# Performance work log

Hardware: AMD Instinct MI355X
Metric: run time of the kernel (lower is better)

Reference implementation:

```python
import jax, jax.numpy as jnp
import numpy as np

K = 256            # number of learned permutations (config['k'])
N = 256            # nb_experts
NOISE_FACTOR = 0.01
TAU_INITIAL = 1e-3
TAU_FINAL = 1e-7
N_ITERS_MIN, N_ITERS_MAX = 20, 150
ITERS_TOTAL = 100 * 1000   # epochs_for_learning_permutation * steps_per_epoch
EPS = 1e-20


def setup_inputs() -> dict:
    key = jax.random.key(0)
    k1, k2 = jax.random.split(key)
    # keras RandomUniform initializer default range is [-0.05, 0.05]
    plw = jax.random.uniform(k1, (K, N, N), jnp.float32, minval=-0.05, maxval=0.05)
    u = jax.random.uniform(k2, (K, N, N), jnp.float32)
    return {"permutation_log_weights": plw, "u": u, "iterations": 5000}


def reference(permutation_log_weights, u, iterations):
    # Linear-in-log10 interpolation of tau and linear interpolation of n_iters
    # over the learning schedule (tfp.math.interp_regular_1d_grid with clamping).
    frac = min(max(float(iterations) / ITERS_TOTAL, 0.0), 1.0)
    log_tau = np.log10(TAU_INITIAL) + frac * (np.log10(TAU_FINAL) - np.log10(TAU_INITIAL))
    tau = np.float32(10.0 ** log_tau)
    n_iters = int(N_ITERS_MIN + frac * (N_ITERS_MAX - N_ITERS_MIN))

    # Gumbel noise from uniform samples, scaled, then temperature scaling.
    noise = -jnp.log(-jnp.log(u + EPS) + EPS) * jnp.float32(NOISE_FACTOR)
    log_alpha = (permutation_log_weights + noise) / tau  # [K, N, N]

    # Log-domain Sinkhorn: alternate row / column log-normalization.
    def step(la, _):
        la = la - jax.scipy.special.logsumexp(la, axis=2, keepdims=True)
        la = la - jax.scipy.special.logsumexp(la, axis=1, keepdims=True)
        return la, None

    log_alpha, _ = jax.lax.scan(step, log_alpha, None, length=n_iters)
    return jnp.exp(log_alpha)  # [K, N, N] near-doubly-stochastic
```

## Files before the change

kernel.cpp:

```cpp
#include <hip/hip_runtime.h>


#define KMAT 256

typedef unsigned uint2_ev __attribute__((ext_vector_type(2)));

__device__ __forceinline__ float fast_exp2(float x) {
#if __has_builtin(__builtin_amdgcn_exp2f)
  return __builtin_amdgcn_exp2f(x);
#else
  return exp2f(x);
#endif
}

__device__ __forceinline__ float fast_log2(float x) {
#if __has_builtin(__builtin_amdgcn_logf)
  return __builtin_amdgcn_logf(x);
#else
  return __log2f(x);
#endif
}

__device__ __forceinline__ float fast_rcp(float x) {
#if __has_builtin(__builtin_amdgcn_rcpf)
  return __builtin_amdgcn_rcpf(x);
#else
  return 1.0f / x;
#endif
}

template <int CTRL>
__device__ __forceinline__ float dpp_movf(float x) {
  return __int_as_float(
      __builtin_amdgcn_update_dpp(0, __float_as_int(x), CTRL, 0xf, 0xf, true));
}

__device__ __forceinline__ float hgroup_max(float x) {
  x = fmaxf(x, dpp_movf<0x121>(x));
  x = fmaxf(x, dpp_movf<0x122>(x));
  x = fmaxf(x, dpp_movf<0x124>(x));
  x = fmaxf(x, dpp_movf<0x128>(x));
#if __has_builtin(__builtin_amdgcn_permlane16_swap)
  uint2_ev r = __builtin_amdgcn_permlane16_swap(
      (unsigned)__float_as_int(x), (unsigned)__float_as_int(x), false, false);
  return fmaxf(__int_as_float((int)r.x), __int_as_float((int)r.y));
#else
  return fmaxf(x, __shfl_xor(x, 16, 64));
#endif
}

__device__ __forceinline__ float hgroup_sum(float x) {
  x += dpp_movf<0x121>(x);
  x += dpp_movf<0x122>(x);
  x += dpp_movf<0x124>(x);
  x += dpp_movf<0x128>(x);
#if __has_builtin(__builtin_amdgcn_permlane16_swap)
  uint2_ev r = __builtin_amdgcn_permlane16_swap(
      (unsigned)__float_as_int(x), (unsigned)__float_as_int(x), false, false);
  return __int_as_float((int)r.x) + __int_as_float((int)r.y);
#else
  return x + __shfl_xor(x, 16, 64);
#endif
}

__device__ __forceinline__ float x32_max(float x) {
#if __has_builtin(__builtin_amdgcn_permlane32_swap)
  uint2_ev r = __builtin_amdgcn_permlane32_swap(
      (unsigned)__float_as_int(x), (unsigned)__float_as_int(x), false, false);
  return fmaxf(__int_as_float((int)r.x), __int_as_float((int)r.y));
#else
  return fmaxf(x, __shfl_xor(x, 32, 64));
#endif
}

__device__ __forceinline__ float x32_sum(float x) {
#if __has_builtin(__builtin_amdgcn_permlane32_swap)
  uint2_ev r = __builtin_amdgcn_permlane32_swap(
      (unsigned)__float_as_int(x), (unsigned)__float_as_int(x), false, false);
  return __int_as_float((int)r.x) + __int_as_float((int)r.y);
#else
  return x + __shfl_xor(x, 32, 64);
#endif
}

__device__ __forceinline__ float gumbel_la(float p, float uv, float scale) {
  float lnu = fast_log2(uv + 1e-20f) * 0.69314718056f;
  float g = fast_log2(1e-20f - lnu) * (-0.0069314718056f);
  return (p + g) * scale;
}

__global__ __launch_bounds__(1024, 1) void lp_sinkhorn_kernel(
    const float* __restrict__ plw, const float* __restrict__ uin,
    const int* __restrict__ itp, float* __restrict__ out) {
  const int k = blockIdx.x;
  const int t = threadIdx.x;
  const int br = t >> 5;
  const int bc = t & 31;
  const int wv = t >> 6;
  const int lane = t & 63;

  __shared__ float red[16 * 256];
  __shared__ float colv[256];

  double frac = (double)itp[0] * 1e-5;
  frac = frac < 0.0 ? 0.0 : (frac > 1.0 ? 1.0 : frac);
  const int n_iters = (int)(20.0 + frac * 130.0);
  const float tauf = (float)exp2((-3.0 - 4.0 * frac) * 3.3219280948873623);
  const float scale = (float)(1.4426950408889634 / (double)tauf);

  float la[8][8];

  const float4* p4 = (const float4*)plw + k * 16384;
  const float4* u4 = (const float4*)uin + k * 16384;
#pragma unroll
  for (int i = 0; i < 8; ++i) {
    const int ridx = ((br << 3) + i) * 64 + (bc << 1);
    float4 p0 = p4[ridx];
    float4 p1 = p4[ridx + 1];
    float4 v0 = u4[ridx];
    float4 v1 = u4[ridx + 1];
    la[i][0] = gumbel_la(p0.x, v0.x, scale);
    la[i][1] = gumbel_la(p0.y, v0.y, scale);
    la[i][2] = gumbel_la(p0.z, v0.z, scale);
    la[i][3] = gumbel_la(p0.w, v0.w, scale);
    la[i][4] = gumbel_la(p1.x, v1.x, scale);
    la[i][5] = gumbel_la(p1.y, v1.y, scale);
    la[i][6] = gumbel_la(p1.z, v1.z, scale);
    la[i][7] = gumbel_la(p1.w, v1.w, scale);
  }

#pragma unroll
  for (int i = 0; i < 8; ++i) {
    float m = la[i][0];
#pragma unroll
    for (int j = 1; j < 8; ++j) m = fmaxf(m, la[i][j]);
    m = hgroup_max(m);
    float s = 0.f;
#pragma unroll
    for (int j = 0; j < 8; ++j) s += fast_exp2(la[i][j] - m);
    s = hgroup_sum(s);
    const float lse = m + fast_log2(s);
#pragma unroll
    for (int j = 0; j < 8; ++j) la[i][j] -= lse;
  }

  {
    float cm[8];
#pragma unroll
    for (int j = 0; j < 8; ++j) {
      float m = la[0][j];
#pragma unroll
      for (int i = 1; i < 8; ++i) m = fmaxf(m, la[i][j]);
      cm[j] = x32_max(m);
    }
    if (lane < 32) {
#pragma unroll
      for (int j = 0; j < 8; ++j) red[wv * 256 + bc + 32 * j] = cm[j];
    }
    __syncthreads();

    float keepm = 0.f;
    if (t < 256) {
      float v[16];
#pragma unroll
      for (int w = 0; w < 16; ++w) v[w] = red[w * 256 + t];
#pragma unroll
      for (int s = 8; s >= 1; s >>= 1)
#pragma unroll
        for (int w = 0; w < s; ++w) v[w] = fmaxf(v[w], v[w + s]);
      keepm = v[0];
      colv[t] = v[0];
    }
    __syncthreads();

#pragma unroll
    for (int j = 0; j < 8; ++j) {
      const float mj = colv[bc + 32 * j];
      float s = 0.f;
#pragma unroll
      for (int i = 0; i < 8; ++i) s += fast_exp2(la[i][j] - mj);
      cm[j] = x32_sum(s);
    }
    __syncthreads();
    if (lane < 32) {
#pragma unroll
      for (int j = 0; j < 8; ++j) red[wv * 256 + bc + 32 * j] = cm[j];
    }
    __syncthreads();

    if (t < 256) {
      float v[16];
#pragma unroll
      for (int w = 0; w < 16; ++w) v[w] = red[w * 256 + t];
#pragma unroll
      for (int s = 8; s >= 1; s >>= 1)
#pragma unroll
        for (int w = 0; w < s; ++w) v[w] += v[w + s];
      colv[t] = keepm + fast_log2(v[0]);
    }
    __syncthreads();

#pragma unroll
    for (int j = 0; j < 8; ++j) {
      const float lse = colv[bc + 32 * j];
#pragma unroll
      for (int i = 0; i < 8; ++i) la[i][j] = fast_exp2(la[i][j] - lse);
    }
  }

  for (int iter = 1; iter < n_iters; ++iter) {
#pragma unroll
    for (int i = 0; i < 8; ++i) {
      float s = la[i][0];
#pragma unroll
      for (int j = 1; j < 8; ++j) s += la[i][j];
      s = hgroup_sum(s);
      const float r = fast_rcp(s);
#pragma unroll
      for (int j = 0; j < 8; ++j) la[i][j] *= r;
    }

    float cs[8];
#pragma unroll
    for (int j = 0; j < 8; ++j) {
      float s = la[0][j];
#pragma unroll
      for (int i = 1; i < 8; ++i) s += la[i][j];
      cs[j] = x32_sum(s);
    }
    if (lane < 32) {
#pragma unroll
      for (int j = 0; j < 8; ++j) red[wv * 256 + bc + 32 * j] = cs[j];
    }
    __syncthreads();

    if (t < 256) {
      float v[16];
#pragma unroll
      for (int w = 0; w < 16; ++w) v[w] = red[w * 256 + t];
#pragma unroll
      for (int s = 8; s >= 1; s >>= 1)
#pragma unroll
        for (int w = 0; w < s; ++w) v[w] += v[w + s];
      colv[t] = fast_rcp(v[0]);
    }
    __syncthreads();

#pragma unroll
    for (int j = 0; j < 8; ++j) {
      const float c = colv[bc + 32 * j];
#pragma unroll
      for (int i = 0; i < 8; ++i) la[i][j] *= c;
    }
  }

  float4* o4 = (float4*)out + k * 16384;
#pragma unroll
  for (int i = 0; i < 8; ++i) {
    const int ridx = ((br << 3) + i) * 64 + (bc << 1);
    float4 a, b;
    a.x = la[i][0]; a.y = la[i][1]; a.z = la[i][2]; a.w = la[i][3];
    b.x = la[i][4]; b.y = la[i][5]; b.z = la[i][6]; b.w = la[i][7];
    o4[ridx] = a;
    o4[ridx + 1] = b;
  }
}

extern "C" void kernel_launch(void* const* d_in, const int* in_sizes, int n_in,
                              void* d_out, int out_size, void* d_ws,
                              size_t ws_size, hipStream_t stream) {
  const float* plw = (const float*)d_in[0];
  const float* u = (const float*)d_in[1];
  const int* iters = (const int*)d_in[2];
  float* out = (float*)d_out;
  (void)in_sizes; (void)n_in; (void)out_size; (void)d_ws; (void)ws_size;
  lp_sinkhorn_kernel<<<dim3(KMAT), dim3(1024), 0, stream>>>(plw, u, iters, out);
}
```

Baseline: 98.40 us.

## Use scaling-vector Sinkhorn form with packed float2 FMAs in iteration loop

Rewrites the Sinkhorn loop so the matrix stays fixed and only row and column scaling vectors (u, v) are updated. Row sums become dot products with v and column sums use the u-weighted matrix, which removes the per-iteration rescaling multiplies of all 64 register elements. The matrix is stored as float2 pairs so the compiler can emit packed FMA/mul instructions. The final u*A*v product is applied at store time. The launch_bounds occupancy hint also changes from 1 to 4, which could alter register allocation.

```diff
diff --git a/kernel.cpp b/kernel.cpp
--- a/kernel.cpp
+++ b/kernel.cpp
@@ -27,6 +27,16 @@
 #else
   return 1.0f / x;
 #endif
+}
+
+__device__ __forceinline__ float2 pk_fma(float2 a, float2 b, float2 c) {
+  return make_float2(fmaf(a.x, b.x, c.x), fmaf(a.y, b.y, c.y));
+}
+__device__ __forceinline__ float2 pk_mul(float2 a, float2 b) {
+  return make_float2(a.x * b.x, a.y * b.y);
+}
+__device__ __forceinline__ float2 pk_sub1(float2 a, float s) {
+  return make_float2(a.x - s, a.y - s);
 }
 
 template <int CTRL>
@@ -89,7 +99,7 @@
   return (p + g) * scale;
 }
 
-__global__ __launch_bounds__(1024, 1) void lp_sinkhorn_kernel(
+__global__ __launch_bounds__(1024, 4) void lp_sinkhorn_kernel(
     const float* __restrict__ plw, const float* __restrict__ uin,
     const int* __restrict__ itp, float* __restrict__ out) {
   const int k = blockIdx.x;
@@ -108,7 +118,7 @@
   const float tauf = (float)exp2((-3.0 - 4.0 * frac) * 3.3219280948873623);
   const float scale = (float)(1.4426950408889634 / (double)tauf);
 
-  float la[8][8];
+  float2 la[8][4];
 
   const float4* p4 = (const float4*)plw + k * 16384;
   const float4* u4 = (const float4*)uin + k * 16384;
@@ -119,43 +129,48 @@
     float4 p1 = p4[ridx + 1];
     float4 v0 = u4[ridx];
     float4 v1 = u4[ridx + 1];
-    la[i][0] = gumbel_la(p0.x, v0.x, scale);
-    la[i][1] = gumbel_la(p0.y, v0.y, scale);
-    la[i][2] = gumbel_la(p0.z, v0.z, scale);
-    la[i][3] = gumbel_la(p0.w, v0.w, scale);
-    la[i][4] = gumbel_la(p1.x, v1.x, scale);
-    la[i][5] = gumbel_la(p1.y, v1.y, scale);
-    la[i][6] = gumbel_la(p1.z, v1.z, scale);
-    la[i][7] = gumbel_la(p1.w, v1.w, scale);
+    la[i][0] = make_float2(gumbel_la(p0.x, v0.x, scale),
+                           gumbel_la(p0.y, v0.y, scale));
+    la[i][1] = make_float2(gumbel_la(p0.z, v0.z, scale),
+                           gumbel_la(p0.w, v0.w, scale));
+    la[i][2] = make_float2(gumbel_la(p1.x, v1.x, scale),
+                           gumbel_la(p1.y, v1.y, scale));
+    la[i][3] = make_float2(gumbel_la(p1.z, v1.z, scale),
+                           gumbel_la(p1.w, v1.w, scale));
   }
 
 #pragma unroll
   for (int i = 0; i < 8; ++i) {
-    float m = la[i][0];
-#pragma unroll
-    for (int j = 1; j < 8; ++j) m = fmaxf(m, la[i][j]);
+    float m = fmaxf(la[i][0].x, la[i][0].y);
+#pragma unroll
+    for (int p = 1; p < 4; ++p) m = fmaxf(m, fmaxf(la[i][p].x, la[i][p].y));
     m = hgroup_max(m);
     float s = 0.f;
 #pragma unroll
-    for (int j = 0; j < 8; ++j) s += fast_exp2(la[i][j] - m);
+    for (int p = 0; p < 4; ++p)
+      s += fast_exp2(la[i][p].x - m) + fast_exp2(la[i][p].y - m);
     s = hgroup_sum(s);
     const float lse = m + fast_log2(s);
 #pragma unroll
-    for (int j = 0; j < 8; ++j) la[i][j] -= lse;
+    for (int p = 0; p < 4; ++p) la[i][p] = pk_sub1(la[i][p], lse);
   }
 
   {
-    float cm[8];
-#pragma unroll
-    for (int j = 0; j < 8; ++j) {
-      float m = la[0][j];
-#pragma unroll
-      for (int i = 1; i < 8; ++i) m = fmaxf(m, la[i][j]);
-      cm[j] = x32_max(m);
+    float2 cm[4];
+#pragma unroll
+    for (int p = 0; p < 4; ++p) {
+      float2 m = la[0][p];
+#pragma unroll
+      for (int i = 1; i < 8; ++i)
+        m = make_float2(fmaxf(m.x, la[i][p].x), fmaxf(m.y, la[i][p].y));
+      cm[p] = make_float2(x32_max(m.x), x32_max(m.y));
     }
     if (lane < 32) {
 #pragma unroll
-      for (int j = 0; j < 8; ++j) red[wv * 256 + bc + 32 * j] = cm[j];
+      for (int p = 0; p < 4; ++p) {
+        red[wv * 256 + bc + 32 * (2 * p)] = cm[p].x;
+        red[wv * 256 + bc + 32 * (2 * p + 1)] = cm[p].y;
+      }
     }
     __syncthreads();
 
@@ -173,18 +188,25 @@
     }
     __syncthreads();
 
-#pragma unroll
-    for (int j = 0; j < 8; ++j) {
-      const float mj = colv[bc + 32 * j];
-      float s = 0.f;
-#pragma unroll
-      for (int i = 0; i < 8; ++i) s += fast_exp2(la[i][j] - mj);
-      cm[j] = x32_sum(s);
+    float2 cs[4];
+#pragma unroll
+    for (int p = 0; p < 4; ++p) {
+      const float2 mj = make_float2(colv[bc + 32 * (2 * p)],
+                                    colv[bc + 32 * (2 * p + 1)]);
+      float2 s = make_float2(0.f, 0.f);
+#pragma unroll
+      for (int i = 0; i < 8; ++i)
+        s = make_float2(s.x + fast_exp2(la[i][p].x - mj.x),
+                        s.y + fast_exp2(la[i][p].y - mj.y));
+      cs[p] = make_float2(x32_sum(s.x), x32_sum(s.y));
     }
     __syncthreads();
     if (lane < 32) {
 #pragma unroll
-      for (int j = 0; j < 8; ++j) red[wv * 256 + bc + 32 * j] = cm[j];
+      for (int p = 0; p < 4; ++p) {
+        red[wv * 256 + bc + 32 * (2 * p)] = cs[p].x;
+        red[wv * 256 + bc + 32 * (2 * p + 1)] = cs[p].y;
+      }
     }
     __syncthreads();
 
@@ -201,36 +223,48 @@
     __syncthreads();
 
 #pragma unroll
-    for (int j = 0; j < 8; ++j) {
-      const float lse = colv[bc + 32 * j];
-#pragma unroll
-      for (int i = 0; i < 8; ++i) la[i][j] = fast_exp2(la[i][j] - lse);
-    }
-  }
+    for (int p = 0; p < 4; ++p) {
+      const float2 lse = make_float2(colv[bc + 32 * (2 * p)],
+                                     colv[bc + 32 * (2 * p + 1)]);
+#pragma unroll
+      for (int i = 0; i < 8; ++i)
+        la[i][p] = make_float2(fast_exp2(la[i][p].x - lse.x),
+                               fast_exp2(la[i][p].y - lse.y));
+    }
+  }
+
+  float uo[8];
+  float2 v2[4] = {make_float2(1.f, 1.f), make_float2(1.f, 1.f),
+                  make_float2(1.f, 1.f), make_float2(1.f, 1.f)};
 
   for (int iter = 1; iter < n_iters; ++iter) {
 #pragma unroll
     for (int i = 0; i < 8; ++i) {
-      float s = la[i][0];
-#pragma unroll
-      for (int j = 1; j < 8; ++j) s += la[i][j];
-      s = hgroup_sum(s);
-      const float r = fast_rcp(s);
-#pragma unroll
-      for (int j = 0; j < 8; ++j) la[i][j] *= r;
-    }
-
-    float cs[8];
-#pragma unroll
-    for (int j = 0; j < 8; ++j) {
-      float s = la[0][j];
-#pragma unroll
-      for (int i = 1; i < 8; ++i) s += la[i][j];
-      cs[j] = x32_sum(s);
-    }
+      float2 acc = pk_mul(la[i][0], v2[0]);
+#pragma unroll
+      for (int p = 1; p < 4; ++p) acc = pk_fma(la[i][p], v2[p], acc);
+      float s = hgroup_sum(acc.x + acc.y);
+      uo[i] = fast_rcp(s);
+    }
+
+    float2 cs[4] = {make_float2(0.f, 0.f), make_float2(0.f, 0.f),
+                    make_float2(0.f, 0.f), make_float2(0.f, 0.f)};
+#pragma unroll
+    for (int i = 0; i < 8; ++i) {
+      const float2 ub = make_float2(uo[i], uo[i]);
+#pragma unroll
+      for (int p = 0; p < 4; ++p) cs[p] = pk_fma(la[i][p], ub, cs[p]);
+    }
+#pragma unroll
+    for (int p = 0; p < 4; ++p)
+      cs[p] = make_float2(x32_sum(cs[p].x), x32_sum(cs[p].y));
+
     if (lane < 32) {
 #pragma unroll
-      for (int j = 0; j < 8; ++j) red[wv * 256 + bc + 32 * j] = cs[j];
+      for (int p = 0; p < 4; ++p) {
+        red[wv * 256 + bc + 32 * (2 * p)] = cs[p].x;
+        red[wv * 256 + bc + 32 * (2 * p + 1)] = cs[p].y;
+      }
     }
     __syncthreads();
 
@@ -247,20 +281,23 @@
     __syncthreads();
 
 #pragma unroll
-    for (int j = 0; j < 8; ++j) {
-      const float c = colv[bc + 32 * j];
-#pragma unroll
-      for (int i = 0; i < 8; ++i) la[i][j] *= c;
-    }
+    for (int p = 0; p < 4; ++p)
+      v2[p] = make_float2(colv[bc + 32 * (2 * p)],
+                          colv[bc + 32 * (2 * p + 1)]);
   }
 
   float4* o4 = (float4*)out + k * 16384;
 #pragma unroll
   for (int i = 0; i < 8; ++i) {
     const int ridx = ((br << 3) + i) * 64 + (bc << 1);
+    const float2 ub = make_float2(uo[i], uo[i]);
+    float2 r0 = pk_mul(pk_mul(la[i][0], ub), v2[0]);
+    float2 r1 = pk_mul(pk_mul(la[i][1], ub), v2[1]);
+    float2 r2 = pk_mul(pk_mul(la[i][2], ub), v2[2]);
+    float2 r3 = pk_mul(pk_mul(la[i][3], ub), v2[3]);
     float4 a, b;
-    a.x = la[i][0]; a.y = la[i][1]; a.z = la[i][2]; a.w = la[i][3];
-    b.x = la[i][4]; b.y = la[i][5]; b.z = la[i][6]; b.w = la[i][7];
+    a.x = r0.x; a.y = r0.y; a.z = r1.x; a.w = r1.y;
+    b.x = r2.x; b.y = r2.y; b.z = r3.x; b.w = r3.y;
     o4[ridx] = a;
     o4[ridx + 1] = b;
   }
```

Result: faster. 94.64 us (-3.8%).
